# Kernel optimization log

Measured on AMD Instinct MI355X. Metric: run time of the kernel, lower is better.

Reference implementation:

```python
import jax, jax.numpy as jnp
import numpy as np

NEG_SLOPE = 0.2
EPS = 1e-16  # PyG softmax denominator epsilon


def gat_conv(x, src, dst, W, att_src, att_dst, bias, concat):
    """One PyG-style GATConv layer (eval mode, self-loops already in src/dst).
    x: [N, F_in]; src/dst: [E]; W: [F_in, H*C]; att_*: [H, C]; bias: [H*C] or [C].
    """
    N = x.shape[0]
    H, C = att_src.shape
    h = (x @ W).reshape(N, H, C)                        # [N,H,C]
    a_s = jnp.sum(h * att_src[None], axis=-1)           # [N,H]
    a_d = jnp.sum(h * att_dst[None], axis=-1)           # [N,H]
    alpha = jax.nn.leaky_relu(a_s[src] + a_d[dst], NEG_SLOPE)  # [E,H]
    # segment softmax over incoming edges of each destination node
    m = jax.ops.segment_max(alpha, dst, num_segments=N)        # [N,H]
    alpha = jnp.exp(alpha - m[dst])
    denom = jax.ops.segment_sum(alpha, dst, num_segments=N)    # [N,H]
    alpha = alpha / (denom[dst] + EPS)
    # attention dropout is identity in eval mode
    out = jax.ops.segment_sum(h[src] * alpha[:, :, None], dst, num_segments=N)  # [N,H,C]
    out = out.reshape(N, H * C) if concat else out.mean(axis=1)
    return out + bias


def setup_inputs() -> dict:
    key = jax.random.key(0)
    ks = jax.random.split(key, 10)
    N, E, F_in, H, C1, F_out = 100000, 1600000, 128, 4, 32, 64
    hid = H * C1
    x = jax.random.normal(ks[0], (N, F_in), dtype=jnp.float32)
    edge_index = jax.random.randint(ks[1], (2, E), 0, N, dtype=jnp.int64)
    s = 1.0 / np.sqrt(F_in)
    W1 = jax.random.uniform(ks[2], (F_in, hid), minval=-s, maxval=s, dtype=jnp.float32)
    att_src1 = jax.random.normal(ks[3], (H, C1), dtype=jnp.float32) * 0.1
    att_dst1 = jax.random.normal(ks[4], (H, C1), dtype=jnp.float32) * 0.1
    b1 = jnp.zeros((hid,), dtype=jnp.float32)
    s2 = 1.0 / np.sqrt(hid)
    W2 = jax.random.uniform(ks[5], (hid, F_out), minval=-s2, maxval=s2, dtype=jnp.float32)
    att_src2 = jax.random.normal(ks[6], (1, F_out), dtype=jnp.float32) * 0.1
    att_dst2 = jax.random.normal(ks[7], (1, F_out), dtype=jnp.float32) * 0.1
    b2 = jnp.zeros((F_out,), dtype=jnp.float32)
    return {"x": x, "edge_index": edge_index,
            "W1": W1, "att_src1": att_src1, "att_dst1": att_dst1, "b1": b1,
            "W2": W2, "att_src2": att_src2, "att_dst2": att_dst2, "b2": b2}


def reference(x, edge_index, W1, att_src1, att_dst1, b1, W2, att_src2, att_dst2, b2):
    N = x.shape[0]
    loops = jnp.arange(N, dtype=edge_index.dtype)
    src = jnp.concatenate([edge_index[0], loops])  # add_self_loops=True (PyG default)
    dst = jnp.concatenate([edge_index[1], loops])
    h = gat_conv(x, src, dst, W1, att_src1, att_dst1, b1, concat=True)
    h = jax.nn.relu(h)  # dropout is identity in eval mode
    return gat_conv(h, src, dst, W2, att_src2, att_dst2, b2, concat=False)
```

## Files before the change

kernel.cpp:

```cpp
#include <hip/hip_runtime.h>
#include <hip/hip_bf16.h>

#define DEV static __device__ __forceinline__

typedef __attribute__((ext_vector_type(4))) float f32x4;
typedef __attribute__((ext_vector_type(8))) short bf16x8;
typedef __attribute__((ext_vector_type(8))) _Float16 half8;
typedef __attribute__((ext_vector_type(2))) _Float16 half2v;
typedef __attribute__((ext_vector_type(8))) unsigned short u16x8;

DEV float leakys(float v) { return v > 0.f ? v : 0.2f * v; }
DEV float4 add4(float4 a, float4 b) { return make_float4(a.x+b.x, a.y+b.y, a.z+b.z, a.w+b.w); }
DEV float4 leaky4(float4 v) { return make_float4(leakys(v.x), leakys(v.y), leakys(v.z), leakys(v.w)); }
DEV float4 exp4(float4 v) { return make_float4(__expf(v.x), __expf(v.y), __expf(v.z), __expf(v.w)); }
DEV float pick4(float4 v, int i) {
    float r = v.x;
    r = (i == 1) ? v.y : r;
    r = (i == 2) ? v.z : r;
    r = (i == 3) ? v.w : r;
    return r;
}

DEV ushort f2bf(float f) {
    union { float f; unsigned u; } v; v.f = f;
    unsigned u = v.u;
    unsigned r = (u + 0x7FFFu + ((u >> 16) & 1u)) >> 16;
    return (ushort)r;
}
DEV float bf2f(ushort h) {
    union { unsigned u; float f; } v; v.u = ((unsigned)h) << 16;
    return v.f;
}
DEV ushort f2h(float f) {
    union { _Float16 h; ushort u; } v;
    v.h = (_Float16)f;
    return v.u;
}
DEV half2v u2h2(ushort2 u) {
    union { ushort2 u; half2v h; } v; v.u = u;
    return v.h;
}

__global__ void prep_w(const float* __restrict__ W, ushort* __restrict__ Wth,
                       ushort* __restrict__ Wtl, int NC) {
    int i = blockIdx.x * 256 + threadIdx.x;
    if (i >= 128 * NC) return;
    int k = i / NC, n = i % NC;
    float v = W[i];
    ushort hi = f2bf(v);
    ushort lo = f2bf(v - bf2f(hi));
    Wth[n * 128 + k] = hi;
    Wtl[n * 128 + k] = lo;
}

template <int NCOLS, bool AH>
__launch_bounds__(256, 2)
__global__ void gemm_mfma(const float* __restrict__ A, const ushort* __restrict__ A16,
                          const ushort* __restrict__ Wth, const ushort* __restrict__ Wtl,
                          ushort* __restrict__ C16,
                          const float* __restrict__ att_s, const float* __restrict__ att_d,
                          float* __restrict__ as_out, float* __restrict__ ad_out, int N,
                          const int* __restrict__ dstIdx, int* __restrict__ bcounts,
                          int E, int nGemmBlocks) {
    constexpr int NT = NCOLS / 64;
    __shared__ ushort Xhi[64 * 128];
    __shared__ ushort Xlo[64 * 128];
    __shared__ float pbs[64][4];
    __shared__ float pbd[64][4];
    const int t = threadIdx.x;

    if (blockIdx.x >= nGemmBlocks) {
        __shared__ int hist[256];
        hist[t] = 0;
        __syncthreads();
        int nb = gridDim.x - nGemmBlocks;
        for (int e = (blockIdx.x - nGemmBlocks) * 256 + t; e < E; e += nb * 256)
            atomicAdd(&hist[dstIdx[e] >> 9], 1);
        __syncthreads();
        int h = hist[t];
        if (h) atomicAdd(&bcounts[t], h);
        return;
    }

    const int wv = t >> 6, l = t & 63;
    const int l15 = l & 15, lhi = l >> 4;
    const int row0 = blockIdx.x * 64;
    const int n0 = wv * 16 * NT;

    if constexpr (!AH) {
        for (int i = t; i < 2048; i += 256) {
            int r = i >> 5, c4 = i & 31;
            int gr = row0 + r;
            float4 v = make_float4(0.f, 0.f, 0.f, 0.f);
            if (gr < N) v = ((const float4*)A)[(size_t)gr * 32 + c4];
            ushort4 hi, lo;
            hi.x = f2bf(v.x); lo.x = f2bf(v.x - bf2f(hi.x));
            hi.y = f2bf(v.y); lo.y = f2bf(v.y - bf2f(hi.y));
            hi.z = f2bf(v.z); lo.z = f2bf(v.z - bf2f(hi.z));
            hi.w = f2bf(v.w); lo.w = f2bf(v.w - bf2f(hi.w));
            int idx = (r * 128 + c4 * 4) ^ ((r & 7) << 3);
            *(ushort4*)&Xhi[idx] = hi;
            *(ushort4*)&Xlo[idx] = lo;
        }
    } else {
        for (int i = t; i < 1024; i += 256) {
            int r = i >> 4, c8 = i & 15;
            int gr = row0 + r;
            half8 v = (half8){0, 0, 0, 0, 0, 0, 0, 0};
            if (gr < N) v = *(const half8*)&A16[(size_t)gr * 128 + c8 * 8];
            u16x8 hi, lo;
#pragma unroll
            for (int j = 0; j < 8; j++) {
                float f = (float)v[j];
                ushort hb = f2bf(f);
                hi[j] = hb;
                lo[j] = f2bf(f - bf2f(hb));
            }
            int idx = (r * 128 + c8 * 8) ^ ((r & 7) << 3);
            *(u16x8*)&Xhi[idx] = hi;
            *(u16x8*)&Xlo[idx] = lo;
        }
    }
    __syncthreads();

    f32x4 acc[4][NT];
#pragma unroll
    for (int mt = 0; mt < 4; mt++)
#pragma unroll
        for (int nt = 0; nt < NT; nt++) acc[mt][nt] = (f32x4){0.f, 0.f, 0.f, 0.f};

#pragma unroll
    for (int ks = 0; ks < 4; ks++) {
        bf16x8 ah[4], al[4];
#pragma unroll
        for (int mt = 0; mt < 4; mt++) {
            int row = mt * 16 + l15;
            int idx = (row * 128 + ks * 32 + lhi * 8) ^ ((row & 7) << 3);
            ah[mt] = *(const bf16x8*)&Xhi[idx];
            al[mt] = *(const bf16x8*)&Xlo[idx];
        }
#pragma unroll
        for (int nt = 0; nt < NT; nt++) {
            size_t wo = (size_t)(n0 + nt * 16 + l15) * 128 + ks * 32 + lhi * 8;
            bf16x8 bh = *(const bf16x8*)&Wth[wo];
            bf16x8 bl = *(const bf16x8*)&Wtl[wo];
#pragma unroll
            for (int mt = 0; mt < 4; mt++) {
                acc[mt][nt] = __builtin_amdgcn_mfma_f32_16x16x32_bf16(ah[mt], bh, acc[mt][nt], 0, 0, 0);
                acc[mt][nt] = __builtin_amdgcn_mfma_f32_16x16x32_bf16(ah[mt], bl, acc[mt][nt], 0, 0, 0);
                acc[mt][nt] = __builtin_amdgcn_mfma_f32_16x16x32_bf16(al[mt], bh, acc[mt][nt], 0, 0, 0);
            }
        }
    }
#pragma unroll
    for (int mt = 0; mt < 4; mt++) {
#pragma unroll
        for (int j = 0; j < 4; j++) {
            int gr = row0 + mt * 16 + lhi * 4 + j;
            if (gr < N) {
#pragma unroll
                for (int nt = 0; nt < NT; nt++)
                    C16[(size_t)gr * NCOLS + n0 + nt * 16 + l15] = f2h(acc[mt][nt][j]);
            }
        }
    }
    if constexpr (NT == 2) {
        float as0 = att_s[n0 + l15],       ad0 = att_d[n0 + l15];
        float as1v = att_s[n0 + 16 + l15], ad1v = att_d[n0 + 16 + l15];
#pragma unroll
        for (int mt = 0; mt < 4; mt++) {
#pragma unroll
            for (int j = 0; j < 4; j++) {
                float ps = acc[mt][0][j] * as0 + acc[mt][1][j] * as1v;
                float pd = acc[mt][0][j] * ad0 + acc[mt][1][j] * ad1v;
#pragma unroll
                for (int o = 1; o < 16; o <<= 1) {
                    ps += __shfl_xor(ps, o);
                    pd += __shfl_xor(pd, o);
                }
                if (l15 == 0) {
                    int gr = row0 + mt * 16 + lhi * 4 + j;
                    if (gr < N) {
                        as_out[gr * 4 + wv] = ps;
                        ad_out[gr * 4 + wv] = pd;
                    }
                }
            }
        }
    } else {
        float as0 = att_s[n0 + l15], ad0 = att_d[n0 + l15];
#pragma unroll
        for (int mt = 0; mt < 4; mt++) {
#pragma unroll
            for (int j = 0; j < 4; j++) {
                float ps = acc[mt][0][j] * as0;
                float pd = acc[mt][0][j] * ad0;
#pragma unroll
                for (int o = 1; o < 16; o <<= 1) {
                    ps += __shfl_xor(ps, o);
                    pd += __shfl_xor(pd, o);
                }
                if (l15 == 0) {
                    int rl = mt * 16 + lhi * 4 + j;
                    pbs[rl][wv] = ps;
                    pbd[rl][wv] = pd;
                }
            }
        }
        __syncthreads();
        if (t < 64) {
            int gr = row0 + t;
            if (gr < N) {
                as_out[gr] = pbs[t][0] + pbs[t][1] + pbs[t][2] + pbs[t][3];
                ad_out[gr] = pbd[t][0] + pbd[t][1] + pbd[t][2] + pbd[t][3];
            }
        }
    }
}

__global__ void bscan(const int* __restrict__ bcounts, int* __restrict__ bbase,
                      int* __restrict__ bcursor, int NB) {
    __shared__ int lds[256];
    int t = threadIdx.x;
    int v = (t < NB) ? bcounts[t] : 0;
    lds[t] = v;
    __syncthreads();
    int val = v;
    for (int o = 1; o < 256; o <<= 1) {
        int other = (t >= o) ? lds[t - o] : 0;
        __syncthreads();
        val += other; lds[t] = val;
        __syncthreads();
    }
    if (t < NB) { bbase[t] = val - v; bcursor[t] = val - v; }
}

__global__ void bscatter(const int* __restrict__ srcIdx, const int* __restrict__ dstIdx,
                         int* __restrict__ bcursor, uint2* __restrict__ ebuf, int E) {
    __shared__ int hist[256];
    __shared__ int gofs[256];
    int t = threadIdx.x;
    hist[t] = 0;
    __syncthreads();
    int e0 = blockIdx.x * 4096;
    int e1 = min(E, e0 + 4096);
    for (int e = e0 + t; e < e1; e += 256)
        atomicAdd(&hist[dstIdx[e] >> 9], 1);
    __syncthreads();
    int h = hist[t];
    if (h) gofs[t] = atomicAdd(&bcursor[t], h);
    __syncthreads();
    hist[t] = 0;
    __syncthreads();
    for (int e = e0 + t; e < e1; e += 256) {
        int d = dstIdx[e];
        int b = d >> 9;
        int r = atomicAdd(&hist[b], 1);
        uint2 v; v.x = (unsigned)srcIdx[e]; v.y = (unsigned)d;
        ebuf[gofs[b] + r] = v;
    }
}

__global__ void bfill(const uint2* __restrict__ ebuf, const int* __restrict__ bbase,
                      int* __restrict__ rowptr, int* __restrict__ esrc,
                      int N, int NB, int E) {
    __shared__ int cnt[512];
    __shared__ int lds[256];
    int b = blockIdx.x, t = threadIdx.x;
    int n0 = b << 9;
    cnt[t] = 0; cnt[t + 256] = 0;
    __syncthreads();
    int e0 = bbase[b];
    int e1 = (b + 1 < NB) ? bbase[b + 1] : E;
    for (int e = e0 + t; e < e1; e += 256)
        atomicAdd(&cnt[ebuf[e].y & 511], 1);
    __syncthreads();
    int c0 = cnt[2 * t], c1 = cnt[2 * t + 1];
    int s = c0 + c1;
    lds[t] = s;
    __syncthreads();
    int val = s;
    for (int o = 1; o < 256; o <<= 1) {
        int other = (t >= o) ? lds[t - o] : 0;
        __syncthreads();
        val += other; lds[t] = val;
        __syncthreads();
    }
    int p = val - s;
    int nrem = N - n0;
    if (2 * t < nrem)     rowptr[n0 + 2 * t]     = e0 + p;
    if (2 * t + 1 < nrem) rowptr[n0 + 2 * t + 1] = e0 + p + c0;
    cnt[2 * t] = p; cnt[2 * t + 1] = p + c0;
    __syncthreads();
    for (int e = e0 + t; e < e1; e += 256) {
        uint2 ed = ebuf[e];
        int r = atomicAdd(&cnt[ed.y & 511], 1);
        esrc[e0 + r] = (int)ed.x;
    }
    if (b == 0 && t == 0) rowptr[N] = E;
}

__launch_bounds__(256)
__global__ void aggregate1(const ushort* __restrict__ h16,
                           const float* __restrict__ as1, const float* __restrict__ ad1,
                           const int* __restrict__ rowptr, const int* __restrict__ esrc,
                           const float* __restrict__ b1, ushort* __restrict__ out1h, int N) {
    __shared__ ushort wbuf[4][4 * 40];
    __shared__ int    sbuf[4][32];
    int wid = threadIdx.x >> 6, lane = threadIdx.x & 63;
    int node = blockIdx.x * 4 + wid;
    if (node >= N) return;
    float4 asn = *(const float4*)&as1[node * 4];
    float4 adn = *(const float4*)&ad1[node * 4];
    float4 selfw = exp4(leaky4(add4(asn, adn)));
    int start = rowptr[node], end = rowptr[node + 1];

    int eidx = lane & 15, hd = lane >> 4;
    float adh1 = pick4(adn, hd);
    int q = lane >> 4, c = lane & 15;
    int hh = c >> 2;
    float esum = 0.f;
    float acc[8] = {0.f, 0.f, 0.f, 0.f, 0.f, 0.f, 0.f, 0.f};

    for (int base = start; base < end; base += 32) {
        int cnt = end - base; if (cnt > 32) cnt = 32;
        int e1i = eidx, e2i = eidx + 16;
        int s1 = 0, s2 = 0; float w1 = 0.f, w2 = 0.f;
        if (e1i < cnt) s1 = esrc[base + e1i];
        if (e2i < cnt) s2 = esrc[base + e2i];
        if (e1i < cnt) w1 = __expf(leakys(as1[s1 * 4 + hd] + adh1));
        if (e2i < cnt) w2 = __expf(leakys(as1[s2 * 4 + hd] + adh1));
        esum += w1 + w2;
        wbuf[wid][hd * 40 + e1i] = f2h(w1);
        wbuf[wid][hd * 40 + e2i] = f2h(w2);
        if (hd == 0) { sbuf[wid][e1i] = s1; sbuf[wid][e2i] = s2; }
#pragma unroll 4
        for (int i = 0; i < cnt; i += 8) {
            int i1 = i + 2 * q;
            int2 ss = *(const int2*)&sbuf[wid][i1];
            half2v wp = u2h2(*(const ushort2*)&wbuf[wid][hh * 40 + i1]);
            half8 hv1 = *(const half8*)&h16[(size_t)ss.x * 128 + c * 8];
            half8 hv2 = *(const half8*)&h16[(size_t)ss.y * 128 + c * 8];
#pragma unroll
            for (int j = 0; j < 8; j++) {
                half2v hp = {hv1[j], hv2[j]};
                acc[j] = __builtin_amdgcn_fdot2(hp, wp, acc[j], false);
            }
        }
    }
#pragma unroll
    for (int o = 1; o < 16; o <<= 1) esum += __shfl_xor(esum, o);
    float denom = __shfl(esum, hh << 4) + pick4(selfw, hh) + 1e-16f;
    float inv = 1.f / denom;
    float sw = pick4(selfw, hh);

#pragma unroll
    for (int j = 0; j < 8; j++) {
        acc[j] += __shfl_xor(acc[j], 16);
        acc[j] += __shfl_xor(acc[j], 32);
    }
    if (q == 0) {
        half8 hs = *(const half8*)&h16[(size_t)node * 128 + c * 8];
        const float* bb = &b1[c * 8];
        half8 ov;
#pragma unroll
        for (int j = 0; j < 8; j++) {
            float oj = fmaxf((acc[j] + sw * (float)hs[j]) * inv + bb[j], 0.f);
            ov[j] = (_Float16)oj;
        }
        *(half8*)&out1h[(size_t)node * 128 + c * 8] = ov;
    }
}

__launch_bounds__(256)
__global__ void aggregate2(const ushort* __restrict__ h16,
                           const float* __restrict__ as2, const float* __restrict__ ad2,
                           const int* __restrict__ rowptr, const int* __restrict__ esrc,
                           const float* __restrict__ b2, float* __restrict__ out, int N) {
    __shared__ ushort wbuf[4][64];
    __shared__ int    sbuf[4][64];
    int wid = threadIdx.x >> 6, lane = threadIdx.x & 63;
    int node = blockIdx.x * 4 + wid;
    if (node >= N) return;
    float adn = ad2[node];
    float selfw = __expf(leakys(as2[node] + adn));
    int start = rowptr[node], end = rowptr[node + 1];

    int q = lane >> 3, c = lane & 7;
    float ssum = 0.f;
    float acc[8] = {0.f, 0.f, 0.f, 0.f, 0.f, 0.f, 0.f, 0.f};

    for (int base = start; base < end; base += 64) {
        int cnt = end - base; if (cnt > 64) cnt = 64;
        int s = 0; float w = 0.f;
        if (lane < cnt) {
            s = esrc[base + lane];
            w = __expf(leakys(as2[s] + adn));
        }
        ssum += w;
        wbuf[wid][lane] = f2h(w);
        sbuf[wid][lane] = s;
#pragma unroll 4
        for (int i = 0; i < cnt; i += 16) {
            int i1 = i + 2 * q;
            int2 ss = *(const int2*)&sbuf[wid][i1];
            half2v wp = u2h2(*(const ushort2*)&wbuf[wid][i1]);
            half8 hv1 = *(const half8*)&h16[(size_t)ss.x * 64 + c * 8];
            half8 hv2 = *(const half8*)&h16[(size_t)ss.y * 64 + c * 8];
#pragma unroll
            for (int j = 0; j < 8; j++) {
                half2v hp = {hv1[j], hv2[j]};
                acc[j] = __builtin_amdgcn_fdot2(hp, wp, acc[j], false);
            }
        }
    }
#pragma unroll
    for (int o = 1; o < 64; o <<= 1) ssum += __shfl_xor(ssum, o);
    float inv = 1.f / (ssum + selfw + 1e-16f);

#pragma unroll
    for (int j = 0; j < 8; j++) {
        acc[j] += __shfl_xor(acc[j], 8);
        acc[j] += __shfl_xor(acc[j], 16);
        acc[j] += __shfl_xor(acc[j], 32);
    }
    if (lane < 8) {
        half8 hs = *(const half8*)&h16[(size_t)node * 64 + c * 8];
        const float* bb = &b2[c * 8];
        float o[8];
#pragma unroll
        for (int j = 0; j < 8; j++)
            o[j] = (acc[j] + selfw * (float)hs[j]) * inv + bb[j];
        float4* op = (float4*)&out[(size_t)node * 64 + c * 8];
        op[0] = make_float4(o[0], o[1], o[2], o[3]);
        op[1] = make_float4(o[4], o[5], o[6], o[7]);
    }
}

extern "C" void kernel_launch(void* const* d_in, const int* in_sizes, int n_in,
                              void* d_out, int out_size, void* d_ws, size_t ws_size,
                              hipStream_t stream) {
    const float* x      = (const float*)d_in[0];
    const int*   ei     = (const int*)d_in[1];
    const float* W1     = (const float*)d_in[2];
    const float* att_s1 = (const float*)d_in[3];
    const float* att_d1 = (const float*)d_in[4];
    const float* b1     = (const float*)d_in[5];
    const float* W2     = (const float*)d_in[6];
    const float* att_s2 = (const float*)d_in[7];
    const float* att_d2 = (const float*)d_in[8];
    const float* b2     = (const float*)d_in[9];

    const int N = in_sizes[0] / 128;
    const int E = in_sizes[1] / 2;
    const int NB = (N + 511) >> 9;

    char* ws = (char*)d_ws;
    size_t off = 0;
    auto alloc = [&](size_t bytes) -> void* {
        off = (off + 255) & ~(size_t)255;
        void* p = ws + off;
        off += bytes;
        return p;
    };
    ushort* h16   = (ushort*)alloc((size_t)N * 128 * 2);
    ushort* out1h = (ushort*)alloc((size_t)N * 128 * 2);
    float* as1    = (float*)alloc((size_t)N * 4 * 4);
    float* ad1    = (float*)alloc((size_t)N * 4 * 4);
    float* as2    = (float*)alloc((size_t)N * 4);
    float* ad2    = (float*)alloc((size_t)N * 4);
    int*   rowptr = (int*)alloc((size_t)(N + 1) * 4);
    int*   esrc   = (int*)alloc((size_t)E * 4);
    int*   bcounts = (int*)alloc(256 * 4);
    int*   bbase   = (int*)alloc(256 * 4);
    int*   bcursor = (int*)alloc(256 * 4);
    ushort* Wt1h  = (ushort*)alloc(128 * 128 * 2);
    ushort* Wt1l  = (ushort*)alloc(128 * 128 * 2);
    ushort* Wt2h  = (ushort*)alloc(64 * 128 * 2);
    ushort* Wt2l  = (ushort*)alloc(64 * 128 * 2);
    ushort* h16b = h16;
    uint2* ebuf = (uint2*)out1h;

    const int* srcIdx = ei;
    const int* dstIdx = ei + E;

    hipMemsetAsync(bcounts, 0, 256 * 4, stream);

    prep_w<<<64, 256, 0, stream>>>(W1, Wt1h, Wt1l, 128);
    prep_w<<<32, 256, 0, stream>>>(W2, Wt2h, Wt2l, 64);

    const int nGemm1 = (N + 63) / 64;
    gemm_mfma<128, false><<<nGemm1 + 512, 256, 0, stream>>>(
        x, nullptr, Wt1h, Wt1l, h16, att_s1, att_d1, as1, ad1, N,
        dstIdx, bcounts, E, nGemm1);

    bscan<<<1, 256, 0, stream>>>(bcounts, bbase, bcursor, NB);
    bscatter<<<(E + 4095) / 4096, 256, 0, stream>>>(srcIdx, dstIdx, bcursor, ebuf, E);
    bfill<<<NB, 256, 0, stream>>>(ebuf, bbase, rowptr, esrc, N, NB, E);

    aggregate1<<<(N + 3) / 4, 256, 0, stream>>>(h16, as1, ad1, rowptr, esrc,
                                                b1, out1h, N);

    const int nGemm2 = (N + 63) / 64;
    gemm_mfma<64, true><<<nGemm2, 256, 0, stream>>>(
        nullptr, out1h, Wt2h, Wt2l, h16b, att_s2, att_d2, as2, ad2, N,
        nullptr, nullptr, 0, nGemm2);

    aggregate2<<<(N + 3) / 4, 256, 0, stream>>>(h16b, as2, ad2, rowptr, esrc,
                                                b2, (float*)d_out, N);
}
```

Before: 246.7 us.

## Fuse edge bucket scatter into GEMM side blocks with fixed-stride bucket buffers

```diff
diff --git a/kernel.cpp b/kernel.cpp
--- a/kernel.cpp
+++ b/kernel.cpp
@@ -8,6 +8,8 @@
 typedef __attribute__((ext_vector_type(8))) _Float16 half8;
 typedef __attribute__((ext_vector_type(2))) _Float16 half2v;
 typedef __attribute__((ext_vector_type(8))) unsigned short u16x8;
+
+#define ESTRIDE 10240
 
 DEV float leakys(float v) { return v > 0.f ? v : 0.2f * v; }
 DEV float4 add4(float4 a, float4 b) { return make_float4(a.x+b.x, a.y+b.y, a.z+b.z, a.w+b.w); }
@@ -60,7 +62,8 @@
                           ushort* __restrict__ C16,
                           const float* __restrict__ att_s, const float* __restrict__ att_d,
                           float* __restrict__ as_out, float* __restrict__ ad_out, int N,
-                          const int* __restrict__ dstIdx, int* __restrict__ bcounts,
+                          const int* __restrict__ srcIdx, const int* __restrict__ dstIdx,
+                          int* __restrict__ bcursor, uint2* __restrict__ ebuf,
                           int E, int nGemmBlocks) {
     constexpr int NT = NCOLS / 64;
     __shared__ ushort Xhi[64 * 128];
@@ -71,14 +74,27 @@
 
     if (blockIdx.x >= nGemmBlocks) {
         __shared__ int hist[256];
+        __shared__ int gofs[256];
         hist[t] = 0;
         __syncthreads();
-        int nb = gridDim.x - nGemmBlocks;
-        for (int e = (blockIdx.x - nGemmBlocks) * 256 + t; e < E; e += nb * 256)
+        int blk = blockIdx.x - nGemmBlocks;
+        int e0 = blk * 4096;
+        int e1 = min(E, e0 + 4096);
+        for (int e = e0 + t; e < e1; e += 256)
             atomicAdd(&hist[dstIdx[e] >> 9], 1);
         __syncthreads();
         int h = hist[t];
-        if (h) atomicAdd(&bcounts[t], h);
+        if (h) gofs[t] = atomicAdd(&bcursor[t], h);
+        __syncthreads();
+        hist[t] = 0;
+        __syncthreads();
+        for (int e = e0 + t; e < e1; e += 256) {
+            int d = dstIdx[e];
+            int b = d >> 9;
+            int r = atomicAdd(&hist[b], 1);
+            uint2 v; v.x = (unsigned)srcIdx[e]; v.y = (unsigned)d;
+            ebuf[(size_t)b * ESTRIDE + gofs[b] + r] = v;
+        }
         return;
     }
 
@@ -218,82 +234,52 @@
     }
 }
 
-__global__ void bscan(const int* __restrict__ bcounts, int* __restrict__ bbase,
-                      int* __restrict__ bcursor, int NB) {
-    __shared__ int lds[256];
-    int t = threadIdx.x;
-    int v = (t < NB) ? bcounts[t] : 0;
-    lds[t] = v;
-    __syncthreads();
-    int val = v;
-    for (int o = 1; o < 256; o <<= 1) {
-        int other = (t >= o) ? lds[t - o] : 0;
-        __syncthreads();
-        val += other; lds[t] = val;
-        __syncthreads();
-    }
-    if (t < NB) { bbase[t] = val - v; bcursor[t] = val - v; }
-}
-
-__global__ void bscatter(const int* __restrict__ srcIdx, const int* __restrict__ dstIdx,
-                         int* __restrict__ bcursor, uint2* __restrict__ ebuf, int E) {
-    __shared__ int hist[256];
-    __shared__ int gofs[256];
-    int t = threadIdx.x;
-    hist[t] = 0;
-    __syncthreads();
-    int e0 = blockIdx.x * 4096;
-    int e1 = min(E, e0 + 4096);
-    for (int e = e0 + t; e < e1; e += 256)
-        atomicAdd(&hist[dstIdx[e] >> 9], 1);
-    __syncthreads();
-    int h = hist[t];
-    if (h) gofs[t] = atomicAdd(&bcursor[t], h);
-    __syncthreads();
-    hist[t] = 0;
-    __syncthreads();
-    for (int e = e0 + t; e < e1; e += 256) {
-        int d = dstIdx[e];
-        int b = d >> 9;
-        int r = atomicAdd(&hist[b], 1);
-        uint2 v; v.x = (unsigned)srcIdx[e]; v.y = (unsigned)d;
-        ebuf[gofs[b] + r] = v;
-    }
-}
-
-__global__ void bfill(const uint2* __restrict__ ebuf, const int* __restrict__ bbase,
+__global__ void bfill(const uint2* __restrict__ ebuf, const int* __restrict__ bcnt,
                       int* __restrict__ rowptr, int* __restrict__ esrc,
                       int N, int NB, int E) {
     __shared__ int cnt[512];
     __shared__ int lds[256];
+    __shared__ int ebase;
     int b = blockIdx.x, t = threadIdx.x;
     int n0 = b << 9;
     cnt[t] = 0; cnt[t + 256] = 0;
-    __syncthreads();
-    int e0 = bbase[b];
-    int e1 = (b + 1 < NB) ? bbase[b + 1] : E;
-    for (int e = e0 + t; e < e1; e += 256)
-        atomicAdd(&cnt[ebuf[e].y & 511], 1);
+    int v = (t < NB) ? bcnt[t] : 0;
+    lds[t] = v;
+    __syncthreads();
+    int val = v;
+    for (int o = 1; o < 256; o <<= 1) {
+        int other = (t >= o) ? lds[t - o] : 0;
+        __syncthreads();
+        val += other; lds[t] = val;
+        __syncthreads();
+    }
+    if (t == b) ebase = val - v;
+    __syncthreads();
+    int e0 = ebase;
+    int mycnt = bcnt[b];
+    const uint2* eb = ebuf + (size_t)b * ESTRIDE;
+    for (int i = t; i < mycnt; i += 256)
+        atomicAdd(&cnt[eb[i].y & 511], 1);
     __syncthreads();
     int c0 = cnt[2 * t], c1 = cnt[2 * t + 1];
     int s = c0 + c1;
     lds[t] = s;
     __syncthreads();
-    int val = s;
+    int val2 = s;
     for (int o = 1; o < 256; o <<= 1) {
         int other = (t >= o) ? lds[t - o] : 0;
         __syncthreads();
-        val += other; lds[t] = val;
-        __syncthreads();
-    }
-    int p = val - s;
+        val2 += other; lds[t] = val2;
+        __syncthreads();
+    }
+    int p = val2 - s;
     int nrem = N - n0;
     if (2 * t < nrem)     rowptr[n0 + 2 * t]     = e0 + p;
     if (2 * t + 1 < nrem) rowptr[n0 + 2 * t + 1] = e0 + p + c0;
     cnt[2 * t] = p; cnt[2 * t + 1] = p + c0;
     __syncthreads();
-    for (int e = e0 + t; e < e1; e += 256) {
-        uint2 ed = ebuf[e];
+    for (int i = t; i < mycnt; i += 256) {
+        uint2 ed = eb[i];
         int r = atomicAdd(&cnt[ed.y & 511], 1);
         esrc[e0 + r] = (int)ed.x;
     }
@@ -471,8 +457,6 @@
     float* ad2    = (float*)alloc((size_t)N * 4);
     int*   rowptr = (int*)alloc((size_t)(N + 1) * 4);
     int*   esrc   = (int*)alloc((size_t)E * 4);
-    int*   bcounts = (int*)alloc(256 * 4);
-    int*   bbase   = (int*)alloc(256 * 4);
     int*   bcursor = (int*)alloc(256 * 4);
     ushort* Wt1h  = (ushort*)alloc(128 * 128 * 2);
     ushort* Wt1l  = (ushort*)alloc(128 * 128 * 2);
@@ -484,19 +468,18 @@
     const int* srcIdx = ei;
     const int* dstIdx = ei + E;
 
-    hipMemsetAsync(bcounts, 0, 256 * 4, stream);
+    hipMemsetAsync(bcursor, 0, 256 * 4, stream);
 
     prep_w<<<64, 256, 0, stream>>>(W1, Wt1h, Wt1l, 128);
     prep_w<<<32, 256, 0, stream>>>(W2, Wt2h, Wt2l, 64);
 
     const int nGemm1 = (N + 63) / 64;
-    gemm_mfma<128, false><<<nGemm1 + 512, 256, 0, stream>>>(
+    const int nScat  = (E + 4095) / 4096;
+    gemm_mfma<128, false><<<nGemm1 + nScat, 256, 0, stream>>>(
         x, nullptr, Wt1h, Wt1l, h16, att_s1, att_d1, as1, ad1, N,
-        dstIdx, bcounts, E, nGemm1);
-
-    bscan<<<1, 256, 0, stream>>>(bcounts, bbase, bcursor, NB);
-    bscatter<<<(E + 4095) / 4096, 256, 0, stream>>>(srcIdx, dstIdx, bcursor, ebuf, E);
-    bfill<<<NB, 256, 0, stream>>>(ebuf, bbase, rowptr, esrc, N, NB, E);
+        srcIdx, dstIdx, bcursor, ebuf, E, nGemm1);
+
+    bfill<<<NB, 256, 0, stream>>>(ebuf, bcursor, rowptr, esrc, N, NB, E);
 
     aggregate1<<<(N + 3) / 4, 256, 0, stream>>>(h16, as1, ad1, rowptr, esrc,
                                                 b1, out1h, N);
@@ -504,7 +487,7 @@
     const int nGemm2 = (N + 63) / 64;
     gemm_mfma<64, true><<<nGemm2, 256, 0, stream>>>(
         nullptr, out1h, Wt2h, Wt2l, h16b, att_s2, att_d2, as2, ad2, N,
-        nullptr, nullptr, 0, nGemm2);
+        nullptr, nullptr, nullptr, nullptr, 0, nGemm2);
 
     aggregate2<<<(N + 3) / 4, 256, 0, stream>>>(h16b, as2, ad2, rowptr, esrc,
                                                 b2, (float*)d_out, N);
```

Measured after the change: 222.4 us (median of 2 runs). 9.8% less time.
